# Kernel tuning notes

Measured on AMD Instinct MI355X. Metric: run time of the kernel, lower is better.

The kernel has to match this reference:

```python
import jax, jax.numpy as jnp
import numpy as np

D_MODEL = 512
NHEAD = 8
HEAD_DIM = D_MODEL // NHEAD
NS = 1  # num_special_tokens


def setup_inputs() -> dict:
    key = jax.random.key(0)
    ks = jax.random.split(key, 12)
    B, N = 8, 1024
    x = jax.random.normal(ks[0], (B, N, D_MODEL), dtype=jnp.float32)
    coords = jax.random.normal(ks[1], (B, N, 3), dtype=jnp.float32) * 5.0
    key_padding_mask = jnp.zeros((B, N), dtype=bool)
    s = 1.0 / np.sqrt(D_MODEL)
    qkv_w = jax.random.normal(ks[2], (3 * D_MODEL, D_MODEL), dtype=jnp.float32) * s
    out_w = jax.random.normal(ks[3], (D_MODEL, D_MODEL), dtype=jnp.float32) * s
    out_b = jnp.zeros((D_MODEL,), dtype=jnp.float32)
    bias_alpha = jnp.ones((1,), dtype=jnp.float32) * 0.5  # nonzero so bias path matters
    w1 = jax.random.normal(ks[4], (NHEAD * 4, 4), dtype=jnp.float32) * 0.5
    b1 = jnp.zeros((NHEAD * 4,), dtype=jnp.float32)
    w2 = jax.random.normal(ks[5], (NHEAD, NHEAD * 4), dtype=jnp.float32) * 0.2
    b2 = jnp.zeros((NHEAD,), dtype=jnp.float32)
    coord_scales = jnp.array([12.0, 12.0, 5.0], dtype=jnp.float32)
    return dict(x=x, coords=coords, key_padding_mask=key_padding_mask,
                qkv_w=qkv_w, out_w=out_w, out_b=out_b, bias_alpha=bias_alpha,
                w1=w1, b1=b1, w2=w2, b2=b2, coord_scales=coord_scales)


def reference(x, coords, key_padding_mask, qkv_w, out_w, out_b, bias_alpha,
              w1, b1, w2, b2, coord_scales):
    B, N, _ = x.shape
    scale = HEAD_DIM ** (-0.5)
    qkv = x @ qkv_w.T  # [B,N,3D]
    q, k, v = jnp.split(qkv, 3, axis=-1)
    def heads(t):
        return t.reshape(B, N, NHEAD, HEAD_DIM).transpose(0, 2, 1, 3)  # [B,H,N,dh]
    q, k, v = heads(q), heads(k), heads(v)

    c = coords / coord_scales  # [B,N,3]
    dpos = c[:, :, None, :] - c[:, None, :, :]  # [B,N,N,3]
    dist = jnp.linalg.norm(dpos, axis=-1, keepdims=True)  # [B,N,N,1]
    feat = jnp.concatenate([dpos, dist], axis=-1)  # [B,N,N,4]
    h = jax.nn.gelu(feat @ w1.T + b1, approximate=False)  # [B,N,N,4H]
    bias = (h @ w2.T + b2).transpose(0, 3, 1, 2)  # [B,H,N,N]
    # zero out bias rows/cols for special tokens
    bias = bias.at[:, :, :NS, :].set(0.0)
    bias = bias.at[:, :, :, :NS].set(0.0)

    dots = jnp.einsum('bhid,bhjd->bhij', q, k) * scale
    logits = dots + bias_alpha * bias
    logits = jnp.where(key_padding_mask[:, None, None, :], -1e30, logits)
    attn = jax.nn.softmax(logits, axis=-1)
    out = jnp.einsum('bhij,bhjd->bhid', attn, v)
    out = out.transpose(0, 2, 1, 3).reshape(B, N, D_MODEL)
    return out @ out_w.T + out_b
```

## Files before the change

### kernel.cpp

```cpp
#include <hip/hip_runtime.h>
#include <hip/hip_bf16.h>
#include <math.h>

#define D_MODEL 512
#define NHEAD   8
#define HEAD_DIM 64
#define BB      8
#define NN      1024
#define NS      1
#define TI      16
#define TJ      32
#define NT      (NN / TJ)
#define FIX_M   10.0f
#define GSTRIDE 40

typedef __attribute__((ext_vector_type(8))) short short8;
typedef __attribute__((ext_vector_type(4))) float floatx4;

__device__ __forceinline__ float gelu_tanh(float x) {
    const float x2 = x * x;
    const float z  = x * fmaf(0.0713548162f, x2, 1.5957691216f);
    const float e  = __expf(z);
    const float r  = __builtin_amdgcn_rcpf(1.0f + e);
    return fmaf(-x, r, x);
}

__device__ __forceinline__ unsigned short f2bf(float f) {
    unsigned u = __float_as_uint(f);
    u = (u + 0x7fffu + ((u >> 16) & 1u)) >> 16;
    return (unsigned short)u;
}

__device__ __forceinline__ uint2 pack4bf(float a, float b, float c, float d) {
    uint2 p;
    p.x = (unsigned)f2bf(a) | ((unsigned)f2bf(b) << 16);
    p.y = (unsigned)f2bf(c) | ((unsigned)f2bf(d) << 16);
    return p;
}

__global__ __launch_bounds__(256)
void gemm_qkv_mfma(const float* __restrict__ A, const float* __restrict__ Bm,
                   unsigned short* __restrict__ Qb, unsigned short* __restrict__ Kb,
                   unsigned short* __restrict__ Vt) {
    __shared__ __align__(16) unsigned short As[128 * GSTRIDE];
    __shared__ __align__(16) unsigned short Bs[128 * GSTRIDE];
    const int tid = threadIdx.x;
    const int bm = blockIdx.y * 128;
    const int bn = blockIdx.x * 128;
    const int wv = tid >> 6, lane = tid & 63, quad = lane >> 4, ln = lane & 15;
    const int wm = (wv >> 1) * 64, wn = (wv & 1) * 64;

    floatx4 acc[4][4];
    #pragma unroll
    for (int i = 0; i < 4; ++i)
        #pragma unroll
        for (int j = 0; j < 4; ++j) acc[i][j] = (floatx4){0.f, 0.f, 0.f, 0.f};

    for (int k0 = 0; k0 < 512; k0 += 32) {
        __syncthreads();
        #pragma unroll
        for (int t = 0; t < 4; ++t) {
            const int c = tid + t * 256;
            const int row = c >> 3, kc = (c & 7) * 4;
            float4 v = *(const float4*)(A + (size_t)(bm + row) * 512 + k0 + kc);
            *(uint2*)&As[row * GSTRIDE + kc] = pack4bf(v.x, v.y, v.z, v.w);
            float4 w = *(const float4*)(Bm + (size_t)(bn + row) * 512 + k0 + kc);
            *(uint2*)&Bs[row * GSTRIDE + kc] = pack4bf(w.x, w.y, w.z, w.w);
        }
        __syncthreads();
        short8 af[4], bf[4];
        #pragma unroll
        for (int mb = 0; mb < 4; ++mb)
            af[mb] = *(const short8*)&As[(wm + mb * 16 + ln) * GSTRIDE + quad * 8];
        #pragma unroll
        for (int nb = 0; nb < 4; ++nb)
            bf[nb] = *(const short8*)&Bs[(wn + nb * 16 + ln) * GSTRIDE + quad * 8];
        #pragma unroll
        for (int mb = 0; mb < 4; ++mb)
            #pragma unroll
            for (int nb = 0; nb < 4; ++nb)
                acc[mb][nb] = __builtin_amdgcn_mfma_f32_16x16x32_bf16(af[mb], bf[nb], acc[mb][nb], 0, 0, 0);
    }

    #pragma unroll
    for (int nb = 0; nb < 4; ++nb) {
        const int n = bn + wn + nb * 16 + ln;
        #pragma unroll
        for (int mb = 0; mb < 4; ++mb) {
            const int m = bm + wm + mb * 16 + quad * 4;
            if (n < 512) {
                #pragma unroll
                for (int r = 0; r < 4; ++r)
                    Qb[(size_t)(m + r) * 512 + n] = f2bf(acc[mb][nb][r] * 0.125f);
            } else if (n < 1024) {
                #pragma unroll
                for (int r = 0; r < 4; ++r)
                    Kb[(size_t)(m + r) * 512 + (n - 512)] = f2bf(acc[mb][nb][r]);
            } else {
                const int bb = m >> 10, tok = m & 1023;
                *(uint2*)(Vt + ((size_t)bb * 512 + (n - 1024)) * NN + tok) =
                    pack4bf(acc[mb][nb][0], acc[mb][nb][1], acc[mb][nb][2], acc[mb][nb][3]);
            }
        }
    }
}

__global__ __launch_bounds__(256)
void gemm_out_mfma(const unsigned short* __restrict__ Ab, const float* __restrict__ Bm,
                   const float* __restrict__ bias, float* __restrict__ C) {
    __shared__ __align__(16) unsigned short As[128 * GSTRIDE];
    __shared__ __align__(16) unsigned short Bs[128 * GSTRIDE];
    const int tid = threadIdx.x;
    const int bm = blockIdx.y * 128;
    const int bn = blockIdx.x * 128;
    const int wv = tid >> 6, lane = tid & 63, quad = lane >> 4, ln = lane & 15;
    const int wm = (wv >> 1) * 64, wn = (wv & 1) * 64;

    floatx4 acc[4][4];
    #pragma unroll
    for (int i = 0; i < 4; ++i)
        #pragma unroll
        for (int j = 0; j < 4; ++j) acc[i][j] = (floatx4){0.f, 0.f, 0.f, 0.f};

    for (int k0 = 0; k0 < 512; k0 += 32) {
        __syncthreads();
        #pragma unroll
        for (int t = 0; t < 4; ++t) {
            const int c = tid + t * 256;
            const int row = c >> 3, kc = (c & 7) * 4;
            *(uint2*)&As[row * GSTRIDE + kc] =
                *(const uint2*)(Ab + (size_t)(bm + row) * 512 + k0 + kc);
            float4 w = *(const float4*)(Bm + (size_t)(bn + row) * 512 + k0 + kc);
            *(uint2*)&Bs[row * GSTRIDE + kc] = pack4bf(w.x, w.y, w.z, w.w);
        }
        __syncthreads();
        short8 af[4], bf[4];
        #pragma unroll
        for (int mb = 0; mb < 4; ++mb)
            af[mb] = *(const short8*)&As[(wm + mb * 16 + ln) * GSTRIDE + quad * 8];
        #pragma unroll
        for (int nb = 0; nb < 4; ++nb)
            bf[nb] = *(const short8*)&Bs[(wn + nb * 16 + ln) * GSTRIDE + quad * 8];
        #pragma unroll
        for (int mb = 0; mb < 4; ++mb)
            #pragma unroll
            for (int nb = 0; nb < 4; ++nb)
                acc[mb][nb] = __builtin_amdgcn_mfma_f32_16x16x32_bf16(af[mb], bf[nb], acc[mb][nb], 0, 0, 0);
    }

    #pragma unroll
    for (int nb = 0; nb < 4; ++nb) {
        const int n = bn + wn + nb * 16 + ln;
        const float bv = bias[n];
        #pragma unroll
        for (int mb = 0; mb < 4; ++mb) {
            const int m = bm + wm + mb * 16 + quad * 4;
            #pragma unroll
            for (int r = 0; r < 4; ++r)
                C[(size_t)(m + r) * 512 + n] = acc[mb][nb][r] + bv;
        }
    }
}

__global__ __launch_bounds__(512, 2)
void attn_kernel(const unsigned short* __restrict__ Qb,
                 const unsigned short* __restrict__ Kb,
                 const unsigned short* __restrict__ Vt,
                 const float* __restrict__ coords,
                 const unsigned char* __restrict__ mask,
                 const float* __restrict__ w1, const float* __restrict__ b1,
                 const float* __restrict__ w2, const float* __restrict__ b2,
                 const float* __restrict__ coord_scales,
                 const float* __restrict__ alpha_p,
                 unsigned short* __restrict__ attn_out) {
    const int b   = blockIdx.y;
    const int i0  = blockIdx.x * TI;
    const int tid = threadIdx.x;
    const int wv  = tid >> 6;
    const int lane = tid & 63;
    const int quad = lane >> 4;
    const int ln   = lane & 15;
    const int h    = wv;

    __shared__ _Float16 bias_s[2][TI][TJ][9];
    __shared__ __align__(16) unsigned short ps[NHEAD][16][40];

    const float alpha = alpha_p[0];
    const float isx = 1.0f / coord_scales[0];
    const float isy = 1.0f / coord_scales[1];
    const float isz = 1.0f / coord_scales[2];

    float cir[2][3];
    #pragma unroll
    for (int g = 0; g < 2; ++g) {
        const float* cp = coords + ((size_t)b * NN + i0 + wv * 2 + g) * 3;
        cir[g][0] = cp[0] * isx; cir[g][1] = cp[1] * isy; cir[g][2] = cp[2] * isz;
    }

    float4 w1r[8]; float b1r[8];
    #pragma unroll
    for (int jj = 0; jj < 8; ++jj) {
        w1r[jj] = *(const float4*)(w1 + (quad * 8 + jj) * 4);
        b1r[jj] = b1[quad * 8 + jj];
    }
    short8 b2f;
    #pragma unroll
    for (int jj = 0; jj < 8; ++jj) {
        const float v = (ln < 8) ? alpha * w2[ln * 32 + quad * 8 + jj] : 0.0f;
        b2f[jj] = (short)f2bf(v);
    }
    const float ab2 = (ln < 8) ? alpha * b2[ln] : 0.0f;

    short8 qf[2];
    #pragma unroll
    for (int kd = 0; kd < 2; ++kd)
        qf[kd] = *(const short8*)(Qb + ((size_t)b * NN + i0 + ln) * 512
                                  + h * 64 + kd * 32 + quad * 8);

    floatx4 oacc[4];
    #pragma unroll
    for (int nd = 0; nd < 4; ++nd) oacc[nd] = (floatx4){0.f, 0.f, 0.f, 0.f};
    float l_part[4];
    #pragma unroll
    for (int r = 0; r < 4; ++r) l_part[r] = 0.f;

    const unsigned char* maskp = mask + (size_t)b * NN;
    float cjx[2], cjy[2], cjz[2];

    #define LOAD_CJ(tt_) do { const int tt = (tt_);                               \
        if (tt < NT) {                                                            \
            const float* cp0 = coords + ((size_t)b * NN + tt * TJ + ln) * 3;      \
            cjx[0] = cp0[0] * isx; cjy[0] = cp0[1] * isy; cjz[0] = cp0[2] * isz;  \
            cjx[1] = cp0[48] * isx; cjy[1] = cp0[49] * isy; cjz[1] = cp0[50] * isz; \
        } } while (0)

    #define MLP_TILE(tt_) do { const int tt = (tt_);                              \
        if (tt < NT) {                                                            \
            const int pbw = tt & 1;                                               \
            const int j0m = tt * TJ;                                              \
            _Pragma("unroll")                                                     \
            for (int g = 0; g < 2; ++g) {                                         \
                const int i = wv * 2 + g;                                         \
                const float cix = cir[g][0], ciy = cir[g][1], ciz = cir[g][2];    \
                const bool irow0 = (i0 + i < NS);                                 \
                _Pragma("unroll")                                                 \
                for (int jh = 0; jh < 2; ++jh) {                                  \
                    const float dx = cix - cjx[jh];                               \
                    const float dy = ciy - cjy[jh];                               \
                    const float dz = ciz - cjz[jh];                               \
                    const float dist = sqrtf(dx * dx + dy * dy + dz * dz);        \
                    float hu[8];                                                  \
                    _Pragma("unroll")                                             \
                    for (int jj = 0; jj < 8; ++jj) {                              \
                        const float4 wa = w1r[jj];                                \
                        float t0v = fmaf(wa.x, dx, fmaf(wa.y, dy,                 \
                                    fmaf(wa.z, dz, fmaf(wa.w, dist, b1r[jj]))));  \
                        hu[jj] = gelu_tanh(t0v);                                  \
                    }                                                             \
                    union { short8 s8; unsigned u4[4]; } H;                       \
                    _Pragma("unroll")                                             \
                    for (int k = 0; k < 4; ++k) {                                 \
                        __hip_bfloat162 t2 = __float22bfloat162_rn(               \
                            make_float2(hu[2 * k], hu[2 * k + 1]));               \
                        H.u4[k] = *(unsigned*)&t2;                                \
                    }                                                             \
                    floatx4 D = __builtin_amdgcn_mfma_f32_16x16x32_bf16(          \
                        H.s8, b2f, (floatx4){0.f, 0.f, 0.f, 0.f}, 0, 0, 0);       \
                    if (ln < 8) {                                                 \
                        _Pragma("unroll")                                         \
                        for (int r = 0; r < 4; ++r) {                             \
                            const int jw = jh * 16 + quad * 4 + r;                \
                            const float val = (irow0 || (j0m + jw < NS))          \
                                              ? 0.0f : (D[r] + ab2);              \
                            bias_s[pbw][i][jw][ln] = (_Float16)val;               \
                        }                                                         \
                    }                                                             \
                }                                                                 \
            }                                                                     \
        } } while (0)

    LOAD_CJ(0);
    MLP_TILE(0);
    __syncthreads();

    for (int jt = 0; jt < NT; ++jt) {
        const int j0 = jt * TJ;
        const int pb = jt & 1;

        short8 kf[4], vf[4];
        {
            const unsigned short* kbase = Kb + ((size_t)b * NN + j0) * 512 + h * 64;
            kf[0] = *(const short8*)(kbase + (size_t)ln * 512 + quad * 8);
            kf[1] = *(const short8*)(kbase + (size_t)ln * 512 + 32 + quad * 8);
            kf[2] = *(const short8*)(kbase + (size_t)(16 + ln) * 512 + quad * 8);
            kf[3] = *(const short8*)(kbase + (size_t)(16 + ln) * 512 + 32 + quad * 8);
            const unsigned short* vbase = Vt + ((size_t)b * 512 + h * 64) * NN + j0 + quad * 8;
            #pragma unroll
            for (int nd = 0; nd < 4; ++nd)
                vf[nd] = *(const short8*)(vbase + (size_t)(nd * 16 + ln) * NN);
        }
        const unsigned char mm0 = maskp[j0 + ln];
        const unsigned char mm1 = maskp[j0 + 16 + ln];

        LOAD_CJ(jt + 1);
        MLP_TILE(jt + 1);

        {
            floatx4 s0 = (floatx4){0.f, 0.f, 0.f, 0.f};
            floatx4 s1 = (floatx4){0.f, 0.f, 0.f, 0.f};
            s0 = __builtin_amdgcn_mfma_f32_16x16x32_bf16(qf[0], kf[0], s0, 0, 0, 0);
            s0 = __builtin_amdgcn_mfma_f32_16x16x32_bf16(qf[1], kf[1], s0, 0, 0, 0);
            s1 = __builtin_amdgcn_mfma_f32_16x16x32_bf16(qf[0], kf[2], s1, 0, 0, 0);
            s1 = __builtin_amdgcn_mfma_f32_16x16x32_bf16(qf[1], kf[3], s1, 0, 0, 0);
            #pragma unroll
            for (int r = 0; r < 4; ++r) {
                const int row = quad * 4 + r;
                float v0 = s0[r] + (float)bias_s[pb][row][ln][h];
                float v1 = s1[r] + (float)bias_s[pb][row][16 + ln][h];
                v0 = mm0 ? -1e30f : v0;
                v1 = mm1 ? -1e30f : v1;
                const float e0 = __expf(v0 - FIX_M);
                const float e1 = __expf(v1 - FIX_M);
                l_part[r] += e0 + e1;
                ps[h][row][ln]      = f2bf(e0);
                ps[h][row][16 + ln] = f2bf(e1);
            }
        }

        __builtin_amdgcn_sched_barrier(0);
        asm volatile("s_waitcnt lgkmcnt(0)" ::: "memory");
        __builtin_amdgcn_sched_barrier(0);

        {
            short8 pa = *(const short8*)&ps[h][ln][quad * 8];
            #pragma unroll
            for (int nd = 0; nd < 4; ++nd)
                oacc[nd] = __builtin_amdgcn_mfma_f32_16x16x32_bf16(pa, vf[nd], oacc[nd], 0, 0, 0);
        }

        __syncthreads();
    }

    {
        float rl[4];
        #pragma unroll
        for (int r = 0; r < 4; ++r) {
            float l = l_part[r];
            l += __shfl_xor(l, 1, 64);
            l += __shfl_xor(l, 2, 64);
            l += __shfl_xor(l, 4, 64);
            l += __shfl_xor(l, 8, 64);
            rl[r] = 1.0f / l;
        }
        #pragma unroll
        for (int nd = 0; nd < 4; ++nd)
            #pragma unroll
            for (int r = 0; r < 4; ++r)
                attn_out[((size_t)b * NN + i0 + quad * 4 + r) * 512
                         + h * 64 + nd * 16 + ln] = f2bf(oacc[nd][r] * rl[r]);
    }
    #undef LOAD_CJ
    #undef MLP_TILE
}

extern "C" void kernel_launch(void* const* d_in, const int* in_sizes, int n_in,
                              void* d_out, int out_size, void* d_ws, size_t ws_size,
                              hipStream_t stream) {
    const float* x        = (const float*)d_in[0];
    const float* coords   = (const float*)d_in[1];
    const unsigned char* kpm = (const unsigned char*)d_in[2];
    const float* qkv_w    = (const float*)d_in[3];
    const float* out_w    = (const float*)d_in[4];
    const float* out_b    = (const float*)d_in[5];
    const float* alpha    = (const float*)d_in[6];
    const float* w1       = (const float*)d_in[7];
    const float* b1       = (const float*)d_in[8];
    const float* w2       = (const float*)d_in[9];
    const float* b2       = (const float*)d_in[10];
    const float* cscales  = (const float*)d_in[11];
    float* out = (float*)d_out;

    const int M = BB * NN;
    unsigned short* Qb = (unsigned short*)d_ws;
    unsigned short* Kb = Qb + (size_t)M * D_MODEL;
    unsigned short* Vt = Kb + (size_t)M * D_MODEL;
    unsigned short* Ao = Vt + (size_t)M * D_MODEL;

    {
        dim3 grid(3 * D_MODEL / 128, M / 128);
        gemm_qkv_mfma<<<grid, 256, 0, stream>>>(x, qkv_w, Qb, Kb, Vt);
    }
    {
        dim3 grid(NN / TI, BB);
        attn_kernel<<<grid, 512, 0, stream>>>(Qb, Kb, Vt, coords, kpm, w1, b1, w2, b2,
                                              cscales, alpha, Ao);
    }
    {
        dim3 grid(D_MODEL / 128, M / 128);
        gemm_out_mfma<<<grid, 256, 0, stream>>>(Ao, out_w, out_b, out);
    }
}
```

Before: 365.3 us.

## Split coordinate-MLP bias into separate kernel writing bf16 bias tensor

Adds a separate kernel that evaluates the pairwise coordinate MLP once and stores the alpha-scaled bias for all heads as a bf16 [B,H,N,N] tensor in workspace. A slimmer attention kernel then reads this bias instead of computing GELU and the MLP inline. The goal is to remove the MLP work and shared-memory staging from the attention inner loop. The cost is a large global write and read of the bias tensor. The split path is used only when the workspace is big enough; otherwise the old fused kernel runs.

```diff
diff --git a/kernel.cpp b/kernel.cpp
--- a/kernel.cpp
+++ b/kernel.cpp
@@ -29,6 +29,10 @@
     unsigned u = __float_as_uint(f);
     u = (u + 0x7fffu + ((u >> 16) & 1u)) >> 16;
     return (unsigned short)u;
+}
+
+__device__ __forceinline__ float bf2f(unsigned short u) {
+    return __uint_as_float(((unsigned)u) << 16);
 }
 
 __device__ __forceinline__ uint2 pack4bf(float a, float b, float c, float d) {
@@ -163,16 +167,220 @@
 }
 
 __global__ __launch_bounds__(512, 2)
-void attn_kernel(const unsigned short* __restrict__ Qb,
-                 const unsigned short* __restrict__ Kb,
-                 const unsigned short* __restrict__ Vt,
-                 const float* __restrict__ coords,
-                 const unsigned char* __restrict__ mask,
-                 const float* __restrict__ w1, const float* __restrict__ b1,
-                 const float* __restrict__ w2, const float* __restrict__ b2,
-                 const float* __restrict__ coord_scales,
-                 const float* __restrict__ alpha_p,
-                 unsigned short* __restrict__ attn_out) {
+void mlp_bias_kernel(const float* __restrict__ coords,
+                     const float* __restrict__ w1, const float* __restrict__ b1,
+                     const float* __restrict__ w2, const float* __restrict__ b2,
+                     const float* __restrict__ coord_scales,
+                     const float* __restrict__ alpha_p,
+                     unsigned short* __restrict__ Bw) {
+    const int jt = blockIdx.x, it = blockIdx.y, b = blockIdx.z;
+    const int i0 = it * TI, j0 = jt * TJ;
+    const int tid = threadIdx.x;
+    const int wv = tid >> 6;
+    const int lane = tid & 63;
+    const int quad = lane >> 4;
+    const int ln   = lane & 15;
+
+    const float alpha = alpha_p[0];
+    const float isx = 1.0f / coord_scales[0];
+    const float isy = 1.0f / coord_scales[1];
+    const float isz = 1.0f / coord_scales[2];
+
+    float cir[2][3];
+    #pragma unroll
+    for (int g = 0; g < 2; ++g) {
+        const float* cp = coords + ((size_t)b * NN + i0 + wv * 2 + g) * 3;
+        cir[g][0] = cp[0] * isx; cir[g][1] = cp[1] * isy; cir[g][2] = cp[2] * isz;
+    }
+    float cjx[2], cjy[2], cjz[2];
+    {
+        const float* cp0 = coords + ((size_t)b * NN + j0 + ln) * 3;
+        cjx[0] = cp0[0] * isx;  cjy[0] = cp0[1] * isy;  cjz[0] = cp0[2] * isz;
+        cjx[1] = cp0[48] * isx; cjy[1] = cp0[49] * isy; cjz[1] = cp0[50] * isz;
+    }
+
+    float4 w1r[8]; float b1r[8];
+    #pragma unroll
+    for (int jj = 0; jj < 8; ++jj) {
+        w1r[jj] = *(const float4*)(w1 + (quad * 8 + jj) * 4);
+        b1r[jj] = b1[quad * 8 + jj];
+    }
+    short8 b2f;
+    #pragma unroll
+    for (int jj = 0; jj < 8; ++jj) {
+        const float v = (ln < 8) ? alpha * w2[ln * 32 + quad * 8 + jj] : 0.0f;
+        b2f[jj] = (short)f2bf(v);
+    }
+    const float ab2 = (ln < 8) ? alpha * b2[ln] : 0.0f;
+
+    #pragma unroll
+    for (int g = 0; g < 2; ++g) {
+        const int i = wv * 2 + g;
+        const float cix = cir[g][0], ciy = cir[g][1], ciz = cir[g][2];
+        const bool irow0 = (i0 + i < NS);
+        #pragma unroll
+        for (int jh = 0; jh < 2; ++jh) {
+            const float dx = cix - cjx[jh];
+            const float dy = ciy - cjy[jh];
+            const float dz = ciz - cjz[jh];
+            const float dist = sqrtf(dx * dx + dy * dy + dz * dz);
+            float hu[8];
+            #pragma unroll
+            for (int jj = 0; jj < 8; ++jj) {
+                const float4 wa = w1r[jj];
+                float t0v = fmaf(wa.x, dx, fmaf(wa.y, dy,
+                            fmaf(wa.z, dz, fmaf(wa.w, dist, b1r[jj]))));
+                hu[jj] = gelu_tanh(t0v);
+            }
+            union { short8 s8; unsigned u4[4]; } H;
+            #pragma unroll
+            for (int k = 0; k < 4; ++k) {
+                __hip_bfloat162 t2 = __float22bfloat162_rn(
+                    make_float2(hu[2 * k], hu[2 * k + 1]));
+                H.u4[k] = *(unsigned*)&t2;
+            }
+            floatx4 D = __builtin_amdgcn_mfma_f32_16x16x32_bf16(
+                H.s8, b2f, (floatx4){0.f, 0.f, 0.f, 0.f}, 0, 0, 0);
+            if (ln < 8) {
+                float v[4];
+                #pragma unroll
+                for (int r = 0; r < 4; ++r) {
+                    const int jw = jh * 16 + quad * 4 + r;
+                    v[r] = (irow0 || (j0 + jw < NS)) ? 0.0f : (D[r] + ab2);
+                }
+                unsigned short* dst = Bw + (((size_t)(b * 8 + ln)) * NN + (i0 + i)) * NN
+                                         + j0 + jh * 16 + quad * 4;
+                *(uint2*)dst = pack4bf(v[0], v[1], v[2], v[3]);
+            }
+        }
+    }
+}
+
+__global__ __launch_bounds__(512, 2)
+void attn_split_kernel(const unsigned short* __restrict__ Qb,
+                       const unsigned short* __restrict__ Kb,
+                       const unsigned short* __restrict__ Vt,
+                       const unsigned short* __restrict__ Bw,
+                       const unsigned char* __restrict__ mask,
+                       unsigned short* __restrict__ attn_out) {
+    const int b   = blockIdx.y;
+    const int i0  = blockIdx.x * TI;
+    const int tid = threadIdx.x;
+    const int wv  = tid >> 6;
+    const int lane = tid & 63;
+    const int quad = lane >> 4;
+    const int ln   = lane & 15;
+    const int h    = wv;
+
+    __shared__ __align__(16) unsigned short ps[NHEAD][16][40];
+
+    short8 qf[2];
+    #pragma unroll
+    for (int kd = 0; kd < 2; ++kd)
+        qf[kd] = *(const short8*)(Qb + ((size_t)b * NN + i0 + ln) * 512
+                                  + h * 64 + kd * 32 + quad * 8);
+
+    floatx4 oacc[4];
+    #pragma unroll
+    for (int nd = 0; nd < 4; ++nd) oacc[nd] = (floatx4){0.f, 0.f, 0.f, 0.f};
+    float l_part[4];
+    #pragma unroll
+    for (int r = 0; r < 4; ++r) l_part[r] = 0.f;
+
+    const unsigned char* maskp = mask + (size_t)b * NN;
+    const unsigned short* bbase = Bw + (((size_t)(b * 8 + h)) * NN + i0) * NN;
+
+    for (int jt = 0; jt < NT; ++jt) {
+        const int j0 = jt * TJ;
+
+        float bv0[4], bv1[4];
+        #pragma unroll
+        for (int r = 0; r < 4; ++r) {
+            const unsigned short* bp = bbase + (size_t)(quad * 4 + r) * NN + j0 + ln;
+            bv0[r] = bf2f(bp[0]);
+            bv1[r] = bf2f(bp[16]);
+        }
+
+        short8 kf[4], vf[4];
+        {
+            const unsigned short* kbase = Kb + ((size_t)b * NN + j0) * 512 + h * 64;
+            kf[0] = *(const short8*)(kbase + (size_t)ln * 512 + quad * 8);
+            kf[1] = *(const short8*)(kbase + (size_t)ln * 512 + 32 + quad * 8);
+            kf[2] = *(const short8*)(kbase + (size_t)(16 + ln) * 512 + quad * 8);
+            kf[3] = *(const short8*)(kbase + (size_t)(16 + ln) * 512 + 32 + quad * 8);
+            const unsigned short* vbase = Vt + ((size_t)b * 512 + h * 64) * NN + j0 + quad * 8;
+            #pragma unroll
+            for (int nd = 0; nd < 4; ++nd)
+                vf[nd] = *(const short8*)(vbase + (size_t)(nd * 16 + ln) * NN);
+        }
+        const unsigned char mm0 = maskp[j0 + ln];
+        const unsigned char mm1 = maskp[j0 + 16 + ln];
+
+        {
+            floatx4 s0 = (floatx4){0.f, 0.f, 0.f, 0.f};
+            floatx4 s1 = (floatx4){0.f, 0.f, 0.f, 0.f};
+            s0 = __builtin_amdgcn_mfma_f32_16x16x32_bf16(qf[0], kf[0], s0, 0, 0, 0);
+            s0 = __builtin_amdgcn_mfma_f32_16x16x32_bf16(qf[1], kf[1], s0, 0, 0, 0);
+            s1 = __builtin_amdgcn_mfma_f32_16x16x32_bf16(qf[0], kf[2], s1, 0, 0, 0);
+            s1 = __builtin_amdgcn_mfma_f32_16x16x32_bf16(qf[1], kf[3], s1, 0, 0, 0);
+            #pragma unroll
+            for (int r = 0; r < 4; ++r) {
+                const int row = quad * 4 + r;
+                float v0 = s0[r] + bv0[r];
+                float v1 = s1[r] + bv1[r];
+                v0 = mm0 ? -1e30f : v0;
+                v1 = mm1 ? -1e30f : v1;
+                const float e0 = __expf(v0 - FIX_M);
+                const float e1 = __expf(v1 - FIX_M);
+                l_part[r] += e0 + e1;
+                ps[h][row][ln]      = f2bf(e0);
+                ps[h][row][16 + ln] = f2bf(e1);
+            }
+        }
+
+        __builtin_amdgcn_sched_barrier(0);
+        asm volatile("s_waitcnt lgkmcnt(0)" ::: "memory");
+        __builtin_amdgcn_sched_barrier(0);
+
+        {
+            short8 pa = *(const short8*)&ps[h][ln][quad * 8];
+            #pragma unroll
+            for (int nd = 0; nd < 4; ++nd)
+                oacc[nd] = __builtin_amdgcn_mfma_f32_16x16x32_bf16(pa, vf[nd], oacc[nd], 0, 0, 0);
+        }
+    }
+
+    {
+        float rl[4];
+        #pragma unroll
+        for (int r = 0; r < 4; ++r) {
+            float l = l_part[r];
+            l += __shfl_xor(l, 1, 64);
+            l += __shfl_xor(l, 2, 64);
+            l += __shfl_xor(l, 4, 64);
+            l += __shfl_xor(l, 8, 64);
+            rl[r] = 1.0f / l;
+        }
+        #pragma unroll
+        for (int nd = 0; nd < 4; ++nd)
+            #pragma unroll
+            for (int r = 0; r < 4; ++r)
+                attn_out[((size_t)b * NN + i0 + quad * 4 + r) * 512
+                         + h * 64 + nd * 16 + ln] = f2bf(oacc[nd][r] * rl[r]);
+    }
+}
+
+__global__ __launch_bounds__(512, 2)
+void attn_fused_kernel(const unsigned short* __restrict__ Qb,
+                       const unsigned short* __restrict__ Kb,
+                       const unsigned short* __restrict__ Vt,
+                       const float* __restrict__ coords,
+                       const unsigned char* __restrict__ mask,
+                       const float* __restrict__ w1, const float* __restrict__ b1,
+                       const float* __restrict__ w2, const float* __restrict__ b2,
+                       const float* __restrict__ coord_scales,
+                       const float* __restrict__ alpha_p,
+                       unsigned short* __restrict__ attn_out) {
     const int b   = blockIdx.y;
     const int i0  = blockIdx.x * TI;
     const int tid = threadIdx.x;
@@ -381,19 +589,35 @@
     float* out = (float*)d_out;
 
     const int M = BB * NN;
+    const size_t seg = (size_t)M * D_MODEL;
     unsigned short* Qb = (unsigned short*)d_ws;
-    unsigned short* Kb = Qb + (size_t)M * D_MODEL;
-    unsigned short* Vt = Kb + (size_t)M * D_MODEL;
-    unsigned short* Ao = Vt + (size_t)M * D_MODEL;
+    unsigned short* Kb = Qb + seg;
+    unsigned short* Vt = Kb + seg;
+    unsigned short* Ao = Vt + seg;
+    unsigned short* Bw = Ao + seg;
+
+    const size_t base_bytes = 4 * seg * 2;
+    const size_t bias_bytes = (size_t)BB * NHEAD * NN * NN * 2;
+    const bool   use_split  = (ws_size >= base_bytes + bias_bytes);
 
     {
         dim3 grid(3 * D_MODEL / 128, M / 128);
         gemm_qkv_mfma<<<grid, 256, 0, stream>>>(x, qkv_w, Qb, Kb, Vt);
     }
-    {
+    if (use_split) {
+        {
+            dim3 grid(NT, NN / TI, BB);
+            mlp_bias_kernel<<<grid, 512, 0, stream>>>(coords, w1, b1, w2, b2,
+                                                      cscales, alpha, Bw);
+        }
+        {
+            dim3 grid(NN / TI, BB);
+            attn_split_kernel<<<grid, 512, 0, stream>>>(Qb, Kb, Vt, Bw, kpm, Ao);
+        }
+    } else {
         dim3 grid(NN / TI, BB);
-        attn_kernel<<<grid, 512, 0, stream>>>(Qb, Kb, Vt, coords, kpm, w1, b1, w2, b2,
-                                              cscales, alpha, Ao);
+        attn_fused_kernel<<<grid, 512, 0, stream>>>(Qb, Kb, Vt, coords, kpm,
+                                                    w1, b1, w2, b2, cscales, alpha, Ao);
     }
     {
         dim3 grid(D_MODEL / 128, M / 128);
```

Result: slower. 458.4 us (+25.5%).
